# Kernel optimization log

Measured on AMD Instinct MI355X. Metric: run time of the kernel, lower is better.

The kernel has to match this reference:

```python
import jax, jax.numpy as jnp
import numpy as np

N_NODES = 100000
N_EDGES = 1600000
D_IN, D_H, D_OUT = 128, 128, 64


def gcn_conv(x, src, dst, W, b, n_nodes):
    """PyG GCNConv (eval): x' = D^{-1/2} (A+I) D^{-1/2} X W + b.
    src/dst already include self-loops."""
    h = x @ W  # [N, d_out] -- transform first (fewer FLOPs when d_out <= d_in)
    deg = jax.ops.segment_sum(jnp.ones_like(dst, dtype=h.dtype), dst, num_segments=n_nodes)
    dinv = jnp.where(deg > 0, jax.lax.rsqrt(deg), 0.0)
    norm = dinv[src] * dinv[dst]  # [E]
    msg = h[src] * norm[:, None]  # gather + scale
    out = jax.ops.segment_sum(msg, dst, num_segments=n_nodes)  # scatter-add
    return out + b


def setup_inputs() -> dict:
    key = jax.random.key(0)
    k = jax.random.split(key, 8)
    x = jax.random.normal(k[0], (N_NODES, D_IN), dtype=jnp.float32)
    edge_index = jax.random.randint(k[1], (2, N_EDGES), 0, N_NODES, dtype=jnp.int32)
    s = 0.1
    W1 = jax.random.normal(k[2], (D_IN, D_H), dtype=jnp.float32) * s
    b1 = jnp.zeros((D_H,), dtype=jnp.float32)
    W2 = jax.random.normal(k[3], (D_H, D_H), dtype=jnp.float32) * s
    b2 = jnp.zeros((D_H,), dtype=jnp.float32)
    W3 = jax.random.normal(k[4], (D_H, D_OUT), dtype=jnp.float32) * s
    b3 = jnp.zeros((D_OUT,), dtype=jnp.float32)
    return {"x": x, "edge_index": edge_index, "W1": W1, "b1": b1,
            "W2": W2, "b2": b2, "W3": W3, "b3": b3}


def reference(x, edge_index, W1, b1, W2, b2, W3, b3):
    n = x.shape[0]
    # add self-loops once (shared by all layers)
    loops = jnp.arange(n, dtype=edge_index.dtype)
    src = jnp.concatenate([edge_index[0], loops])
    dst = jnp.concatenate([edge_index[1], loops])
    h = gcn_conv(x, src, dst, W1, b1, n)
    h = jax.nn.relu(h)  # dropout = identity in eval mode
    h = gcn_conv(h, src, dst, W2, b2, n)
    h = jax.nn.relu(h)
    out = gcn_conv(h, src, dst, W3, b3, n)
    return out
```

## Files before the change

### kernel.cpp

```cpp
#include <hip/hip_runtime.h>
#include <hip/hip_fp16.h>

#define N_NODES 100000
#define N_EDGES 1600000
#define NBUCKET 196
#define CAP     8960
#define EPB     6250

typedef _Float16 half8 __attribute__((ext_vector_type(8)));
typedef float float4v __attribute__((ext_vector_type(4)));

__launch_bounds__(256)
__global__ void k_partition(const int* __restrict__ src, const int* __restrict__ dst,
                            int* __restrict__ bcur, int* __restrict__ ebuf, int E) {
    __shared__ int hist[200];
    __shared__ int basebkt[200];
    const int tid = threadIdx.x;
    if (tid < 200) hist[tid] = 0;
    __syncthreads();
    const int e0 = blockIdx.x * EPB, e1 = min(e0 + EPB, E);
    for (int e = e0 + tid; e < e1; e += 256) atomicAdd(&hist[dst[e] >> 9], 1);
    __syncthreads();
    if (tid < NBUCKET) {
        int h = hist[tid];
        basebkt[tid] = tid * CAP + (h ? atomicAdd(&bcur[tid], h) : 0);
    }
    __syncthreads();
    if (tid < 200) hist[tid] = 0;
    __syncthreads();
    for (int e = e0 + tid; e < e1; e += 256) {
        int d = dst[e];
        int bk = d >> 9;
        int o = atomicAdd(&hist[bk], 1);
        ebuf[basebkt[bk] + o] = (src[e] << 9) | (d & 511);
    }
}

__launch_bounds__(256)
__global__ void k_bsort(const int* __restrict__ ebuf, const int* __restrict__ bcur,
                        int* __restrict__ adj, int* __restrict__ stv,
                        int* __restrict__ deg, float* __restrict__ dinv, int N) {
    __shared__ int cnt[512];
    __shared__ int offs[512];
    const int b = blockIdx.x;
    const int tid = threadIdx.x;
    const int base = b * CAP;
    const int n_b = min(bcur[b], CAP);
    const int node0 = b << 9;
    cnt[tid] = 0; cnt[tid + 256] = 0;
    __syncthreads();
    for (int i = tid; i < n_b; i += 256)
        atomicAdd(&cnt[ebuf[base + i] & 511], 1);
    __syncthreads();
    if (tid < 64) {
        int v[8], tot = 0;
#pragma unroll
        for (int j = 0; j < 8; ++j) { int t = cnt[tid * 8 + j]; v[j] = tot; tot += t; }
        int inc = tot;
#pragma unroll
        for (int d = 1; d < 64; d <<= 1) {
            int u = __shfl_up(inc, d, 64);
            if (tid >= d) inc += u;
        }
        const int excl = inc - tot;
#pragma unroll
        for (int j = 0; j < 8; ++j) offs[tid * 8 + j] = excl + v[j];
    }
    __syncthreads();
#pragma unroll
    for (int h = 0; h < 2; ++h) {
        int local = tid + h * 256;
        int node = node0 + local;
        if (node < N) {
            stv[node] = base + offs[local];
            deg[node] = cnt[local];
            dinv[node] = rsqrtf((float)(cnt[local] + 1));
        }
    }
    __syncthreads();
    for (int i = tid; i < n_b; i += 256) {
        int pk = ebuf[base + i];
        int pos = atomicAdd(&offs[pk & 511], 1);
        adj[base + pos] = pk >> 9;
    }
}

__global__ void k_wswz_all(const float* __restrict__ W1, const float* __restrict__ W2,
                           const float* __restrict__ W3, _Float16* __restrict__ wz1,
                           _Float16* __restrict__ wz2, _Float16* __restrict__ wz3,
                           int* __restrict__ bcur) {
    if (blockIdx.x == 0) bcur[threadIdx.x] = 0;
    int t = blockIdx.x * 256 + threadIdx.x;
    const float* W; _Float16* wsz; int BN;
    if (t < 2048)      { W = W1; wsz = wz1; BN = 128; }
    else if (t < 4096) { W = W2; wsz = wz2; BN = 128; t -= 2048; }
    else if (t < 5120) { W = W3; wsz = wz3; BN = 64;  t -= 4096; }
    else return;
    const int l = t & 63;
    const int kblk = (t >> 6) & 3;
    const int nt = t >> 8;
    const int krow = kblk * 32 + ((l >> 4) << 3);
    const int col = nt * 16 + (l & 15);
    _Float16 v[8];
#pragma unroll
    for (int j = 0; j < 8; ++j) v[j] = (_Float16)W[(krow + j) * BN + col];
    *(uint4*)&wsz[t << 3] = *(uint4*)v;
}

template <int BN, bool AFP16>
__launch_bounds__(256, 4)
__global__ void k_gemm_mfma(const void* __restrict__ Xv, const _Float16* __restrict__ wsz,
                            const float* __restrict__ dinv, __half* __restrict__ out, int N) {
    constexpr int NT = BN / 16;
    constexpr int PAD = 8;
    __shared__ __align__(16) _Float16 smem[BN * 128];

    const int tid = threadIdx.x;
    for (int i = tid; i < BN * 16; i += 256)
        *(uint4*)&smem[i << 3] = *(const uint4*)&wsz[i << 3];

    const int w = tid >> 6;
    const int lane = tid & 63;
    const int q = lane >> 4;
    const int m = lane & 15;
    const int row0 = blockIdx.x * 64;
    const int arow = row0 + w * 16 + m;
    const int arowc = arow < N ? arow : N - 1;

    float4v acc[NT];
#pragma unroll
    for (int nt = 0; nt < NT; ++nt) acc[nt] = (float4v){0.f, 0.f, 0.f, 0.f};

    __syncthreads();

#pragma unroll
    for (int kblk = 0; kblk < 4; ++kblk) {
        half8 af;
        if constexpr (AFP16) {
            const _Float16* A = (const _Float16*)Xv + (size_t)arowc * 128 + (q << 3);
            af = *(const half8*)(A + kblk * 32);
        } else {
            const float* A = (const float*)Xv + (size_t)arowc * 128 + (q << 3);
            float4 a0 = *(const float4*)(A + kblk * 32);
            float4 a1 = *(const float4*)(A + kblk * 32 + 4);
            af[0] = (_Float16)a0.x; af[1] = (_Float16)a0.y;
            af[2] = (_Float16)a0.z; af[3] = (_Float16)a0.w;
            af[4] = (_Float16)a1.x; af[5] = (_Float16)a1.y;
            af[6] = (_Float16)a1.z; af[7] = (_Float16)a1.w;
        }
#pragma unroll
        for (int nt = 0; nt < NT; ++nt) {
            half8 bf = *(const half8*)&smem[(((nt << 2) + kblk) << 9) + (lane << 3)];
            acc[nt] = __builtin_amdgcn_mfma_f32_16x16x32_f16(af, bf, acc[nt], 0, 0, 0);
        }
    }

    float s[4];
#pragma unroll
    for (int r = 0; r < 4; ++r) {
        int rr = row0 + w * 16 + q * 4 + r;
        s[r] = dinv[rr < N ? rr : N - 1];
    }
    __syncthreads();
    _Float16* eb = smem;
#pragma unroll
    for (int nt = 0; nt < NT; ++nt)
#pragma unroll
        for (int r = 0; r < 4; ++r)
            eb[(w * 16 + q * 4 + r) * (BN + PAD) + nt * 16 + m] = (_Float16)(acc[nt][r] * s[r]);
    __syncthreads();
    constexpr int CPR = BN / 8;
    for (int i = tid; i < 64 * CPR; i += 256) {
        int row = i / CPR;
        int cf = (i % CPR) * 8;
        if (row0 + row < N)
            *(uint4*)&out[(size_t)(row0 + row) * BN + cf] = *(uint4*)&eb[row * (BN + PAD) + cf];
    }
}

template <bool RELU>
__launch_bounds__(256)
__global__ void k_agg128(const __half* __restrict__ tp, const int* __restrict__ adj,
                         const int* __restrict__ startv, const int* __restrict__ deg,
                         const float* __restrict__ dinv, const float* __restrict__ bias,
                         _Float16* __restrict__ out, int N) {
    const int node = (blockIdx.x << 2) + (threadIdx.x >> 6);
    const int lane = threadIdx.x & 63;
    if (node >= N) return;
    const int s = startv[node];
    const int cnt = deg[node];
    const float di = dinv[node];
    const int g = lane >> 4;
    const int sl = lane & 15;
    const uint4* rowb = (const uint4*)tp;

    float acc[8] = {0.f, 0.f, 0.f, 0.f, 0.f, 0.f, 0.f, 0.f};
    auto addrow = [&](uint4 v) {
        float2 f0 = __half22float2(*(__half2*)&v.x);
        float2 f1 = __half22float2(*(__half2*)&v.y);
        float2 f2 = __half22float2(*(__half2*)&v.z);
        float2 f3 = __half22float2(*(__half2*)&v.w);
        acc[0] += f0.x; acc[1] += f0.y; acc[2] += f1.x; acc[3] += f1.y;
        acc[4] += f2.x; acc[5] += f2.y; acc[6] += f3.x; acc[7] += f3.y;
    };
    if (g == 0) addrow(rowb[(size_t)node * 16 + sl]);

    int e = 0;
    for (; e + 16 <= cnt; e += 16) {
        int j[4];
#pragma unroll
        for (int u = 0; u < 4; ++u) j[u] = adj[s + e + 4 * u + g];
        uint4 v[4];
#pragma unroll
        for (int u = 0; u < 4; ++u) v[u] = rowb[(size_t)j[u] * 16 + sl];
#pragma unroll
        for (int u = 0; u < 4; ++u) addrow(v[u]);
    }
    for (; e + 4 <= cnt; e += 4)
        addrow(rowb[(size_t)adj[s + e + g] * 16 + sl]);
    if (e + g < cnt)
        addrow(rowb[(size_t)adj[s + e + g] * 16 + sl]);

#pragma unroll
    for (int i = 0; i < 8; ++i) {
        acc[i] += __shfl_xor(acc[i], 32);
        acc[i] += __shfl_xor(acc[i], 16);
    }
    if (g == 0) {
        float4 b0 = *(const float4*)&bias[sl * 8];
        float4 b1 = *(const float4*)&bias[sl * 8 + 4];
        float o[8];
        o[0] = di * acc[0] + b0.x; o[1] = di * acc[1] + b0.y;
        o[2] = di * acc[2] + b0.z; o[3] = di * acc[3] + b0.w;
        o[4] = di * acc[4] + b1.x; o[5] = di * acc[5] + b1.y;
        o[6] = di * acc[6] + b1.z; o[7] = di * acc[7] + b1.w;
        if (RELU)
#pragma unroll
            for (int i = 0; i < 8; ++i) o[i] = fmaxf(o[i], 0.f);
        __half2 ov[4];
#pragma unroll
        for (int i = 0; i < 4; ++i) ov[i] = __floats2half2_rn(o[2 * i], o[2 * i + 1]);
        *(uint4*)&out[(size_t)node * 128 + sl * 8] = *(uint4*)ov;
    }
}

__launch_bounds__(256)
__global__ void k_agg64(const __half* __restrict__ tp, const int* __restrict__ adj,
                        const int* __restrict__ startv, const int* __restrict__ deg,
                        const float* __restrict__ dinv, const float* __restrict__ bias,
                        float* __restrict__ out, int N) {
    const int node = (blockIdx.x << 2) + (threadIdx.x >> 6);
    const int lane = threadIdx.x & 63;
    if (node >= N) return;
    const int s = startv[node];
    const int cnt = deg[node];
    const float di = dinv[node];
    const int g = lane >> 4;
    const int sl = lane & 15;
    const uint2* rowb = (const uint2*)tp;

    float acc[4] = {0.f, 0.f, 0.f, 0.f};
    auto addrow = [&](uint2 v) {
        float2 f0 = __half22float2(*(__half2*)&v.x);
        float2 f1 = __half22float2(*(__half2*)&v.y);
        acc[0] += f0.x; acc[1] += f0.y; acc[2] += f1.x; acc[3] += f1.y;
    };
    if (g == 0) addrow(rowb[(size_t)node * 16 + sl]);

    int e = 0;
    for (; e + 16 <= cnt; e += 16) {
        int j[4];
#pragma unroll
        for (int u = 0; u < 4; ++u) j[u] = adj[s + e + 4 * u + g];
        uint2 v[4];
#pragma unroll
        for (int u = 0; u < 4; ++u) v[u] = rowb[(size_t)j[u] * 16 + sl];
#pragma unroll
        for (int u = 0; u < 4; ++u) addrow(v[u]);
    }
    for (; e + 4 <= cnt; e += 4)
        addrow(rowb[(size_t)adj[s + e + g] * 16 + sl]);
    if (e + g < cnt)
        addrow(rowb[(size_t)adj[s + e + g] * 16 + sl]);

#pragma unroll
    for (int i = 0; i < 4; ++i) {
        acc[i] += __shfl_xor(acc[i], 32);
        acc[i] += __shfl_xor(acc[i], 16);
    }
    if (g == 0) {
        float4 bb = *(const float4*)&bias[sl * 4];
        float4 o;
        o.x = di * acc[0] + bb.x; o.y = di * acc[1] + bb.y;
        o.z = di * acc[2] + bb.z; o.w = di * acc[3] + bb.w;
        *(float4*)&out[(size_t)node * 64 + sl * 4] = o;
    }
}

extern "C" void kernel_launch(void* const* d_in, const int* in_sizes, int n_in,
                              void* d_out, int out_size, void* d_ws, size_t ws_size,
                              hipStream_t stream) {
    const float* x  = (const float*)d_in[0];
    const int*   ei = (const int*)d_in[1];
    const float* W1 = (const float*)d_in[2];
    const float* b1 = (const float*)d_in[3];
    const float* W2 = (const float*)d_in[4];
    const float* b2 = (const float*)d_in[5];
    const float* W3 = (const float*)d_in[6];
    const float* b3 = (const float*)d_in[7];
    float* out = (float*)d_out;
    const int* src = ei;
    const int* dst = ei + N_EDGES;

    char* p = (char*)d_ws;
    __half* tp      = (__half*)p;    p += (size_t)N_NODES * 128 * 2;
    _Float16* hbuf  = (_Float16*)p;  p += (size_t)N_NODES * 128 * 2;
    int*   deg  = (int*)p;    p += (size_t)N_NODES * 4;
    float* dinv = (float*)p;  p += (size_t)N_NODES * 4;
    int*   stv  = (int*)p;    p += (size_t)N_NODES * 4;
    int*   bCur = (int*)p;    p += 1024;
    int*   adj  = (int*)p;    p += (size_t)NBUCKET * CAP * 4 + 16384;
    _Float16* wz1 = (_Float16*)p; p += 16384 * 2;
    _Float16* wz2 = (_Float16*)p; p += 16384 * 2;
    _Float16* wz3 = (_Float16*)p; p += 8192 * 2;
    size_t need = (size_t)(p - (char*)d_ws);
    if (ws_size < need) return;

    int* ebuf = (int*)tp;

    k_wswz_all<<<20, 256, 0, stream>>>(W1, W2, W3, wz1, wz2, wz3, bCur);
    k_partition<<<256, 256, 0, stream>>>(src, dst, bCur, ebuf, N_EDGES);
    k_bsort<<<NBUCKET, 256, 0, stream>>>(ebuf, bCur, adj, stv, deg, dinv, N_NODES);

    const int gb = (N_NODES + 63) / 64;
    const int ab = (N_NODES + 3) / 4;
    k_gemm_mfma<128, false><<<gb, 256, 0, stream>>>(x, wz1, dinv, tp, N_NODES);
    k_agg128<true><<<ab, 256, 0, stream>>>(tp, adj, stv, deg, dinv, b1, hbuf, N_NODES);
    k_gemm_mfma<128, true><<<gb, 256, 0, stream>>>(hbuf, wz2, dinv, tp, N_NODES);
    k_agg128<true><<<ab, 256, 0, stream>>>(tp, adj, stv, deg, dinv, b2, hbuf, N_NODES);
    k_gemm_mfma<64, true><<<gb, 256, 0, stream>>>(hbuf, wz3, dinv, tp, N_NODES);
    k_agg64<<<ab, 256, 0, stream>>>(tp, adj, stv, deg, dinv, b3, out, N_NODES);
}
```

Before: 362.2 us.

## Merge weight swizzle into partition kernel and use fma_mix accumulation in aggregation

The weight-swizzle kernel is folded into the partition launch as extra blocks, and the bucket-counter reset becomes a hipMemsetAsync, trading one kernel launch for a memset. The aggregation kernels now accumulate fp16 neighbour rows with v_fma_mix_f32 inline asm instead of separate convert-and-add, and they load adjacency indices with nontemporal loads. The remainder loop after the 16-edge unrolled loop is replaced by fixed 8-edge and 4-edge steps, which exposes more loads in flight at once. The memset still costs a launch, and the gains in the aggregation kernels depend on whether they are limited by ALU work or by gather bandwidth.

```diff
diff --git a/kernel.cpp b/kernel.cpp
--- a/kernel.cpp
+++ b/kernel.cpp
@@ -10,9 +10,39 @@
 typedef _Float16 half8 __attribute__((ext_vector_type(8)));
 typedef float float4v __attribute__((ext_vector_type(4)));
 
+__device__ __forceinline__ void fmix_lo(float& a, unsigned int w, float one) {
+    asm("v_fma_mix_f32 %0, %1, %2, %0 op_sel:[0,0,0] op_sel_hi:[1,0,0]"
+        : "+v"(a) : "v"(w), "v"(one));
+}
+__device__ __forceinline__ void fmix_hi(float& a, unsigned int w, float one) {
+    asm("v_fma_mix_f32 %0, %1, %2, %0 op_sel:[1,0,0] op_sel_hi:[1,0,0]"
+        : "+v"(a) : "v"(w), "v"(one));
+}
+
 __launch_bounds__(256)
-__global__ void k_partition(const int* __restrict__ src, const int* __restrict__ dst,
-                            int* __restrict__ bcur, int* __restrict__ ebuf, int E) {
+__global__ void k_part_wswz(const int* __restrict__ src, const int* __restrict__ dst,
+                            int* __restrict__ bcur, int* __restrict__ ebuf, int E,
+                            const float* __restrict__ W1, const float* __restrict__ W2,
+                            const float* __restrict__ W3, _Float16* __restrict__ wz1,
+                            _Float16* __restrict__ wz2, _Float16* __restrict__ wz3) {
+    if (blockIdx.x >= 256) {
+        int t = (blockIdx.x - 256) * 256 + threadIdx.x;
+        const float* W; _Float16* wsz; int BN;
+        if (t < 2048)      { W = W1; wsz = wz1; BN = 128; }
+        else if (t < 4096) { W = W2; wsz = wz2; BN = 128; t -= 2048; }
+        else if (t < 5120) { W = W3; wsz = wz3; BN = 64;  t -= 4096; }
+        else return;
+        const int l = t & 63;
+        const int kblk = (t >> 6) & 3;
+        const int nt = t >> 8;
+        const int krow = kblk * 32 + ((l >> 4) << 3);
+        const int col = nt * 16 + (l & 15);
+        _Float16 v[8];
+#pragma unroll
+        for (int j = 0; j < 8; ++j) v[j] = (_Float16)W[(krow + j) * BN + col];
+        *(uint4*)&wsz[t << 3] = *(uint4*)v;
+        return;
+    }
     __shared__ int hist[200];
     __shared__ int basebkt[200];
     const int tid = threadIdx.x;
@@ -83,28 +113,6 @@
         int pos = atomicAdd(&offs[pk & 511], 1);
         adj[base + pos] = pk >> 9;
     }
-}
-
-__global__ void k_wswz_all(const float* __restrict__ W1, const float* __restrict__ W2,
-                           const float* __restrict__ W3, _Float16* __restrict__ wz1,
-                           _Float16* __restrict__ wz2, _Float16* __restrict__ wz3,
-                           int* __restrict__ bcur) {
-    if (blockIdx.x == 0) bcur[threadIdx.x] = 0;
-    int t = blockIdx.x * 256 + threadIdx.x;
-    const float* W; _Float16* wsz; int BN;
-    if (t < 2048)      { W = W1; wsz = wz1; BN = 128; }
-    else if (t < 4096) { W = W2; wsz = wz2; BN = 128; t -= 2048; }
-    else if (t < 5120) { W = W3; wsz = wz3; BN = 64;  t -= 4096; }
-    else return;
-    const int l = t & 63;
-    const int kblk = (t >> 6) & 3;
-    const int nt = t >> 8;
-    const int krow = kblk * 32 + ((l >> 4) << 3);
-    const int col = nt * 16 + (l & 15);
-    _Float16 v[8];
-#pragma unroll
-    for (int j = 0; j < 8; ++j) v[j] = (_Float16)W[(krow + j) * BN + col];
-    *(uint4*)&wsz[t << 3] = *(uint4*)v;
 }
 
 template <int BN, bool AFP16>
@@ -190,18 +198,17 @@
     const int s = startv[node];
     const int cnt = deg[node];
     const float di = dinv[node];
+    const float one = 1.0f;
     const int g = lane >> 4;
     const int sl = lane & 15;
     const uint4* rowb = (const uint4*)tp;
 
     float acc[8] = {0.f, 0.f, 0.f, 0.f, 0.f, 0.f, 0.f, 0.f};
     auto addrow = [&](uint4 v) {
-        float2 f0 = __half22float2(*(__half2*)&v.x);
-        float2 f1 = __half22float2(*(__half2*)&v.y);
-        float2 f2 = __half22float2(*(__half2*)&v.z);
-        float2 f3 = __half22float2(*(__half2*)&v.w);
-        acc[0] += f0.x; acc[1] += f0.y; acc[2] += f1.x; acc[3] += f1.y;
-        acc[4] += f2.x; acc[5] += f2.y; acc[6] += f3.x; acc[7] += f3.y;
+        fmix_lo(acc[0], v.x, one); fmix_hi(acc[1], v.x, one);
+        fmix_lo(acc[2], v.y, one); fmix_hi(acc[3], v.y, one);
+        fmix_lo(acc[4], v.z, one); fmix_hi(acc[5], v.z, one);
+        fmix_lo(acc[6], v.w, one); fmix_hi(acc[7], v.w, one);
     };
     if (g == 0) addrow(rowb[(size_t)node * 16 + sl]);
 
@@ -209,17 +216,30 @@
     for (; e + 16 <= cnt; e += 16) {
         int j[4];
 #pragma unroll
-        for (int u = 0; u < 4; ++u) j[u] = adj[s + e + 4 * u + g];
+        for (int u = 0; u < 4; ++u) j[u] = __builtin_nontemporal_load(&adj[s + e + 4 * u + g]);
         uint4 v[4];
 #pragma unroll
         for (int u = 0; u < 4; ++u) v[u] = rowb[(size_t)j[u] * 16 + sl];
 #pragma unroll
         for (int u = 0; u < 4; ++u) addrow(v[u]);
     }
-    for (; e + 4 <= cnt; e += 4)
-        addrow(rowb[(size_t)adj[s + e + g] * 16 + sl]);
+    if (e + 8 <= cnt) {
+        int j[2];
+#pragma unroll
+        for (int u = 0; u < 2; ++u) j[u] = __builtin_nontemporal_load(&adj[s + e + 4 * u + g]);
+        uint4 v[2];
+#pragma unroll
+        for (int u = 0; u < 2; ++u) v[u] = rowb[(size_t)j[u] * 16 + sl];
+#pragma unroll
+        for (int u = 0; u < 2; ++u) addrow(v[u]);
+        e += 8;
+    }
+    if (e + 4 <= cnt) {
+        addrow(rowb[(size_t)__builtin_nontemporal_load(&adj[s + e + g]) * 16 + sl]);
+        e += 4;
+    }
     if (e + g < cnt)
-        addrow(rowb[(size_t)adj[s + e + g] * 16 + sl]);
+        addrow(rowb[(size_t)__builtin_nontemporal_load(&adj[s + e + g]) * 16 + sl]);
 
 #pragma unroll
     for (int i = 0; i < 8; ++i) {
@@ -255,15 +275,15 @@
     const int s = startv[node];
     const int cnt = deg[node];
     const float di = dinv[node];
+    const float one = 1.0f;
     const int g = lane >> 4;
     const int sl = lane & 15;
     const uint2* rowb = (const uint2*)tp;
 
     float acc[4] = {0.f, 0.f, 0.f, 0.f};
     auto addrow = [&](uint2 v) {
-        float2 f0 = __half22float2(*(__half2*)&v.x);
-        float2 f1 = __half22float2(*(__half2*)&v.y);
-        acc[0] += f0.x; acc[1] += f0.y; acc[2] += f1.x; acc[3] += f1.y;
+        fmix_lo(acc[0], v.x, one); fmix_hi(acc[1], v.x, one);
+        fmix_lo(acc[2], v.y, one); fmix_hi(acc[3], v.y, one);
     };
     if (g == 0) addrow(rowb[(size_t)node * 16 + sl]);
 
@@ -271,17 +291,30 @@
     for (; e + 16 <= cnt; e += 16) {
         int j[4];
 #pragma unroll
-        for (int u = 0; u < 4; ++u) j[u] = adj[s + e + 4 * u + g];
+        for (int u = 0; u < 4; ++u) j[u] = __builtin_nontemporal_load(&adj[s + e + 4 * u + g]);
         uint2 v[4];
 #pragma unroll
         for (int u = 0; u < 4; ++u) v[u] = rowb[(size_t)j[u] * 16 + sl];
 #pragma unroll
         for (int u = 0; u < 4; ++u) addrow(v[u]);
     }
-    for (; e + 4 <= cnt; e += 4)
-        addrow(rowb[(size_t)adj[s + e + g] * 16 + sl]);
+    if (e + 8 <= cnt) {
+        int j[2];
+#pragma unroll
+        for (int u = 0; u < 2; ++u) j[u] = __builtin_nontemporal_load(&adj[s + e + 4 * u + g]);
+        uint2 v[2];
+#pragma unroll
+        for (int u = 0; u < 2; ++u) v[u] = rowb[(size_t)j[u] * 16 + sl];
+#pragma unroll
+        for (int u = 0; u < 2; ++u) addrow(v[u]);
+        e += 8;
+    }
+    if (e + 4 <= cnt) {
+        addrow(rowb[(size_t)__builtin_nontemporal_load(&adj[s + e + g]) * 16 + sl]);
+        e += 4;
+    }
     if (e + g < cnt)
-        addrow(rowb[(size_t)adj[s + e + g] * 16 + sl]);
+        addrow(rowb[(size_t)__builtin_nontemporal_load(&adj[s + e + g]) * 16 + sl]);
 
 #pragma unroll
     for (int i = 0; i < 4; ++i) {
@@ -328,8 +361,9 @@
 
     int* ebuf = (int*)tp;
 
-    k_wswz_all<<<20, 256, 0, stream>>>(W1, W2, W3, wz1, wz2, wz3, bCur);
-    k_partition<<<256, 256, 0, stream>>>(src, dst, bCur, ebuf, N_EDGES);
+    hipMemsetAsync(bCur, 0, 1024, stream);
+    k_part_wswz<<<276, 256, 0, stream>>>(src, dst, bCur, ebuf, N_EDGES,
+                                         W1, W2, W3, wz1, wz2, wz3);
     k_bsort<<<NBUCKET, 256, 0, stream>>>(ebuf, bCur, adj, stv, deg, dinv, N_NODES);
 
     const int gb = (N_NODES + 63) / 64;
```

After: 368.4 us. Within noise of the previous version (+1.7%).
